# Kernel tuning notes

Measured on AMD Instinct MI355X. Metric: run time of the kernel, lower is better.

Reference implementation:

```python
import jax, jax.numpy as jnp
import numpy as np

NUM_CODES = 4096
CODE_DIM = 512
BETA = 0.25
EPS = 1e-5


def setup_inputs() -> dict:
    key = jax.random.key(0)
    k1, k2 = jax.random.split(key)
    z_e = jax.random.normal(k1, (8, 2048, CODE_DIM), dtype=jnp.float32)
    mask = jnp.ones((8, 2048), dtype=bool)
    # torch init: uniform(-1/num_codes, 1/num_codes)
    codebook = jax.random.uniform(
        k2, (NUM_CODES, CODE_DIM), dtype=jnp.float32,
        minval=-1.0 / NUM_CODES, maxval=1.0 / NUM_CODES)
    return {"z_e": z_e, "mask": mask, "codebook": codebook}


def _l2norm(x, eps=1e-8):
    # matches F.normalize: x / norm.clamp_min(eps)
    n = jnp.sqrt(jnp.sum(x * x, axis=-1, keepdims=True))
    return x / jnp.maximum(n, eps)


def reference(z_e, mask, codebook):
    """Eval-mode forward of VectorQuantizerEMA (no gumbel noise, no code
    dropout, no EMA/restart buffer updates -- those only run in training)."""
    B, L, C = z_e.shape
    K = codebook.shape[0]
    flat = z_e.reshape(-1, C)                      # [N, C]
    fmask = mask.reshape(-1)                       # [N] bool
    mf = fmask.astype(flat.dtype)

    # cosine similarity logits  [N, K]
    logits = _l2norm(flat) @ _l2norm(codebook).T
    logits = jnp.clip(
        jnp.nan_to_num(logits, nan=0.0, posinf=1e9, neginf=-1e9), -60.0, 60.0)

    hard_idx = jnp.argmax(logits, axis=1)          # [N]

    # hard one-hot quantization == gather of codebook rows; masked rows -> 0
    z_q_flat = codebook[hard_idx] * mf[:, None]
    z_q = z_q_flat.reshape(B, L, C)
    z_q_st = z_e + jax.lax.stop_gradient(z_q - z_e)

    m = mf.reshape(B, L, 1)
    valid = jnp.maximum(jnp.sum(m), 1.0)
    commitment_loss = jnp.sum((z_q - jax.lax.stop_gradient(z_e)) ** 2 * m) / valid
    vq_loss = BETA * commitment_loss

    # perplexity over valid assignments (bincount)
    counts = jax.ops.segment_sum(mf, hard_idx, num_segments=K)
    probs = counts / (jnp.sum(counts) + EPS)
    perplexity = jnp.exp(-jnp.sum(probs * jnp.log(probs + EPS)))

    return (z_q, z_q_st, hard_idx.reshape(B, L), vq_loss,
            commitment_loss, perplexity)
```

## Files before the change

kernel.cpp:

```cpp
#include <hip/hip_runtime.h>

typedef __attribute__((ext_vector_type(4))) float f32x4_t;
typedef __attribute__((ext_vector_type(8))) short bf16x8_t;

#define NROWS 16384
#define NCODES 4096
#define DIM 512
#define DELTA 0.005f

#define WS_A      0u
#define WS_B      16777216u
#define WS_TOPE   20971520u
#define WS_COUNTS 37748736u
#define WS_FLAGS  37765120u
#define WS_IDX    37765184u
#define WS_CPART  39206976u

#define OUT_ZQ      0
#define OUT_ZQST    8388608
#define OUT_IDX     16777216
#define OUT_VQ      16793600
#define OUT_COMMIT  16793601
#define OUT_PERP    16793602

__device__ __forceinline__ unsigned short f2bf(float x) {
  unsigned u = __builtin_bit_cast(unsigned, x);
  unsigned r = (u + 0x7FFFu + ((u >> 16) & 1u)) >> 16;
  return (unsigned short)r;
}
__device__ __forceinline__ unsigned hz(unsigned x) {
  return (x - 0x01010101u) & ~x & 0x80808080u;
}
__device__ __forceinline__ unsigned swz64(int r, int u) {
  return (unsigned)(r * 128 + ((u ^ (r & 7)) << 4));
}

__global__ void prep_kernel(const float* __restrict__ z, const float* __restrict__ cb,
                            const uint4* __restrict__ mk,
                            unsigned char* __restrict__ Aws, unsigned char* __restrict__ Bws,
                            unsigned* __restrict__ counts, unsigned* __restrict__ flags) {
  if (blockIdx.x < 16) {
    counts[blockIdx.x * 256 + threadIdx.x] = 0;
  }
  if (blockIdx.x == 0) {
    if (threadIdx.x < 4) flags[threadIdx.x] = 0;
    __syncthreads();
    unsigned f = 0;
    for (int i = threadIdx.x; i < 1024; i += 256) {
      uint4 v = mk[i];
      f |= hz(v.x) | hz(v.y) | hz(v.z) | hz(v.w);
    }
    if (f) atomicOr(&flags[0], 1u);
  }
  const int wv = threadIdx.x >> 6, lane = threadIdx.x & 63;
  const int row = blockIdx.x * 4 + wv;
  if (row >= NROWS + NCODES) return;
  const bool isA = row < NROWS;
  const int lrow = isA ? row : row - NROWS;
  const float* src = (isA ? z : cb) + (size_t)lrow * DIM;
  f32x4_t a = *(const f32x4_t*)(src + lane * 8);
  f32x4_t b = *(const f32x4_t*)(src + lane * 8 + 4);
  double s = 0.0;
#pragma unroll
  for (int e = 0; e < 4; ++e) s += (double)a[e] * a[e] + (double)b[e] * b[e];
#pragma unroll
  for (int off = 1; off < 64; off <<= 1) s += __shfl_xor(s, off);
  const float inv = (float)(1.0 / fmax(sqrt(s), 1e-8));
  union { unsigned short u[8]; uint4 v; } H;
#pragma unroll
  for (int e = 0; e < 4; ++e) {
    H.u[e] = f2bf(a[e] * inv);
    H.u[4 + e] = f2bf(b[e] * inv);
  }
  const int tb = lrow >> 7, rr = lrow & 127;
  const int st = lane >> 3, u = lane & 7;
  unsigned char* chunk = (isA ? Aws : Bws) + ((size_t)tb * 8 + st) * 16384;
  *(uint4*)(chunk + swz64(rr, u)) = H.v;
}

__global__ __launch_bounds__(256, 4) void gemm_p1_kernel(
    const unsigned char* __restrict__ Aws, const unsigned char* __restrict__ Bws,
    float4* __restrict__ topE) {
  __align__(16) __shared__ unsigned char smem[32768];

  const int tid = threadIdx.x;
  const int bid = blockIdx.x;
  const int xcd = bid & 7, q = bid >> 3;
  const int rb = xcd * 16 + (q >> 3), cg = q & 7;
  const int wave = tid >> 6, lane = tid & 63;
  const int wr = wave >> 1, wc = wave & 1;
  const int kg = lane >> 4, lr = lane & 15;

  const unsigned char* Ach = Aws + (size_t)rb * 8 * 16384;

  auto issue_stage = [&](const unsigned char* Asrc, const unsigned char* Bsrc) {
#pragma unroll
    for (int i = 0; i < 8; ++i) {
      const int j = wave * 8 + i;
      const unsigned char* sp = (j < 16) ? (Asrc + (size_t)j * 1024 + lane * 16)
                                         : (Bsrc + (size_t)(j - 16) * 1024 + lane * 16);
      __builtin_amdgcn_global_load_lds(
          (const __attribute__((address_space(1))) void*)sp,
          (__attribute__((address_space(3))) void*)(smem + j * 1024), 16, 0, 0);
    }
  };

  for (int ct = 0; ct < 4; ++ct) {
    const int ctile = cg * 4 + ct;
    const int code0 = ctile * 128;
    const unsigned char* Bch = Bws + (size_t)ctile * 8 * 16384;

    f32x4_t acc[4][4];
#pragma unroll
    for (int m = 0; m < 4; ++m)
#pragma unroll
      for (int n = 0; n < 4; ++n) acc[m][n] = (f32x4_t){0.f, 0.f, 0.f, 0.f};

    for (int st = 0; st < 8; ++st) {
      if (!(st == 0 && ct > 0))
        issue_stage(Ach + (size_t)st * 16384, Bch + (size_t)st * 16384);
      __syncthreads();

#pragma unroll
      for (int kk = 0; kk < 2; ++kk) {
        bf16x8_t ah[4], bh[4];
        const int u = kk * 4 + kg;
#pragma unroll
        for (int m = 0; m < 4; ++m) {
          const int r = wr * 64 + m * 16 + lr;
          ah[m] = *(const bf16x8_t*)(smem + swz64(r, u));
        }
#pragma unroll
        for (int n = 0; n < 4; ++n) {
          const int r = wc * 64 + n * 16 + lr;
          bh[n] = *(const bf16x8_t*)(smem + 16384 + swz64(r, u));
        }
#pragma unroll
        for (int m = 0; m < 4; ++m)
#pragma unroll
          for (int n = 0; n < 4; ++n)
            acc[m][n] = __builtin_amdgcn_mfma_f32_16x16x32_bf16(ah[m], bh[n], acc[m][n], 0, 0, 0);
      }
      __syncthreads();
    }

    if (ct < 3)
      issue_stage(Ach, Bws + (size_t)(ctile + 1) * 8 * 16384);

#pragma unroll
    for (int m = 0; m < 4; ++m) {
#pragma unroll
      for (int j = 0; j < 4; ++j) {
        float v1 = -3e38f, v2 = -3e38f; int i1 = 0, i2 = 0;
#pragma unroll
        for (int n = 0; n < 4; ++n) {
          float v = acc[m][n][j];
          int gc = code0 + wc * 64 + n * 16 + lr;
          if (v > v1) { v2 = v1; i2 = i1; v1 = v; i1 = gc; }
          else if (v > v2) { v2 = v; i2 = gc; }
        }
#pragma unroll
        for (int mask = 1; mask <= 8; mask <<= 1) {
          float ov1 = __shfl_xor(v1, mask); int oi1 = __shfl_xor(i1, mask);
          float ov2 = __shfl_xor(v2, mask); int oi2 = __shfl_xor(i2, mask);
          bool of = (ov1 > v1) || (ov1 == v1 && oi1 < i1);
          float w1 = of ? ov1 : v1;  int k1 = of ? oi1 : i1;
          float lv = of ? v1 : ov1;  int li = of ? i1 : oi1;
          float sv = of ? ov2 : v2;  int si = of ? oi2 : i2;
          bool lw = (lv > sv) || (lv == sv && li < si);
          v1 = w1; i1 = k1;
          v2 = lw ? lv : sv; i2 = lw ? li : si;
        }
        if (lr == m * 4 + j) {
          const int row = rb * 128 + wr * 64 + m * 16 + kg * 4 + j;
          topE[(size_t)row * 64 + ctile * 2 + wc] =
              make_float4(v1, __builtin_bit_cast(float, i1), v2, __builtin_bit_cast(float, i2));
        }
      }
    }
  }
}

__global__ void resolve_referee_kernel(const float* __restrict__ z, const float* __restrict__ cb,
                                       const float4* __restrict__ topE, int* __restrict__ idxf) {
  const int wv = threadIdx.x >> 6, lane = threadIdx.x & 63;
  const int row = blockIdx.x * 4 + wv;
  const float4 qv = topE[(size_t)row * 64 + lane];
  const int myi = __builtin_bit_cast(int, qv.y);
  float bv = qv.x; int bidx = myi;
#pragma unroll
  for (int off = 1; off < 64; off <<= 1) {
    float ov = __shfl_xor(bv, off);
    int oi = __shfl_xor(bidx, off);
    if (ov > bv || (ov == bv && oi < bidx)) { bv = ov; bidx = oi; }
  }
  const float T = bv - 2.0f * DELTA;
  const unsigned long long cmask = __ballot(qv.x >= T);
  const unsigned long long smask = __ballot(qv.z >= T);
  if (__popcll(cmask) <= 1 && smask == 0ull) {
    if (lane == 0) idxf[row] = bidx;
    return;
  }
  const float* zr = z + (size_t)row * DIM + lane * 8;
  double zv[8];
#pragma unroll
  for (int j = 0; j < 8; ++j) zv[j] = (double)zr[j];
  double bs = -1e300; int bi = 1 << 30;
  auto score2 = [&](int k0, int k1) {
    const float* c0 = cb + (size_t)k0 * DIM + lane * 8;
    const float* c1 = cb + (size_t)((k1 < 0) ? k0 : k1) * DIM + lane * 8;
    double d0 = 0, n0 = 0, d1 = 0, n1 = 0;
#pragma unroll
    for (int j = 0; j < 8; ++j) {
      double a = c0[j]; d0 += zv[j] * a; n0 += a * a;
      double b = c1[j]; d1 += zv[j] * b; n1 += b * b;
    }
#pragma unroll
    for (int off = 1; off < 64; off <<= 1) {
      d0 += __shfl_xor(d0, off); n0 += __shfl_xor(n0, off);
      d1 += __shfl_xor(d1, off); n1 += __shfl_xor(n1, off);
    }
    double s0 = d0 / sqrt(n0);
    if (s0 > bs || (s0 == bs && k0 < bi)) { bs = s0; bi = k0; }
    if (k1 >= 0) {
      double s1 = d1 / sqrt(n1);
      if (s1 > bs || (s1 == bs && k1 < bi)) { bs = s1; bi = k1; }
    }
  };
  unsigned long long em = cmask & ~smask;
  while (em) {
    const int h0 = __builtin_ctzll(em); em &= em - 1;
    const int c0 = __shfl(myi, h0);
    int c1 = -1;
    if (em) { const int h1 = __builtin_ctzll(em); em &= em - 1; c1 = __shfl(myi, h1); }
    score2(c0, c1);
  }
  unsigned long long m = smask;
  while (m) {
    const int g = __builtin_ctzll(m); m &= m - 1;
    const int base = g * 64;
    for (int k = 0; k < 64; k += 2) score2(base + k, base + k + 1);
  }
  if (lane == 0) idxf[row] = bi;
}

__global__ void outputs_kernel(const float* __restrict__ z, const float* __restrict__ cb,
                               const unsigned char* __restrict__ mask8, const int* __restrict__ mask32,
                               const unsigned* __restrict__ flags, const int* __restrict__ idxf,
                               float* __restrict__ out, unsigned* __restrict__ counts,
                               double* __restrict__ cpart) {
  __shared__ double wsum[4];
  const int wv = threadIdx.x >> 6, lane = threadIdx.x & 63;
  const int row = blockIdx.x * 4 + wv;
  int idx = idxf[row];
  idx = (idx < 0) ? 0 : ((idx > NCODES - 1) ? NCODES - 1 : idx);
  const int mi = flags[0] ? (mask32[row] != 0) : (mask8[row] != 0);
  const float mf = mi ? 1.0f : 0.0f;
  const float* zr = z + (size_t)row * DIM;
  const float* cr = cb + (size_t)idx * DIM;
  double cs = 0.0;
#pragma unroll
  for (int h = 0; h < 2; ++h) {
    const int j = h * 256 + lane * 4;
    f32x4_t c  = *(const f32x4_t*)(cr + j);
    f32x4_t ze = *(const f32x4_t*)(zr + j);
    f32x4_t zq, zs;
#pragma unroll
    for (int e = 0; e < 4; ++e) {
      float qv = c[e] * mf;
      float d = qv - ze[e];
      zq[e] = qv;
      zs[e] = ze[e] + d;
      cs += (double)(d * d) * mf;
    }
    *(f32x4_t*)(out + OUT_ZQ   + (size_t)row * DIM + j) = zq;
    *(f32x4_t*)(out + OUT_ZQST + (size_t)row * DIM + j) = zs;
  }
#pragma unroll
  for (int off = 32; off; off >>= 1) cs += __shfl_down(cs, off);
  if (lane == 0) {
    wsum[wv] = cs;
    out[OUT_IDX + row] = (float)idx;
    if (mi) atomicAdd(&counts[idx], 1u);
  }
  __syncthreads();
  if (threadIdx.x == 0) cpart[blockIdx.x] = wsum[0] + wsum[1] + wsum[2] + wsum[3];
}

__global__ void finalize_kernel(const double* __restrict__ cpart, const unsigned* __restrict__ counts,
                                float* __restrict__ out) {
  __shared__ double sd[256];
  const int t = threadIdx.x;
  double s = 0;
  for (int i = t; i < 4096; i += 256) s += cpart[i];
  sd[t] = s; __syncthreads();
  for (int off = 128; off; off >>= 1) { if (t < off) sd[t] += sd[t + off]; __syncthreads(); }
  const double commit_sum = sd[0];
  __syncthreads();
  double c = 0;
  for (int i = t; i < 4096; i += 256) c += (double)counts[i];
  sd[t] = c; __syncthreads();
  for (int off = 128; off; off >>= 1) { if (t < off) sd[t] += sd[t + off]; __syncthreads(); }
  const double totc = sd[0];
  __syncthreads();
  const double denom = totc + 1e-5;
  double ent = 0;
  for (int i = t; i < 4096; i += 256) {
    double p = (double)counts[i] / denom;
    ent -= p * log(p + 1e-5);
  }
  sd[t] = ent; __syncthreads();
  for (int off = 128; off; off >>= 1) { if (t < off) sd[t] += sd[t + off]; __syncthreads(); }
  if (t == 0) {
    const double valid = fmax(totc, 1.0);
    const double commitment = commit_sum / valid;
    out[OUT_VQ]     = (float)(0.25 * commitment);
    out[OUT_COMMIT] = (float)commitment;
    out[OUT_PERP]   = (float)exp(sd[0]);
  }
}

extern "C" void kernel_launch(void* const* d_in, const int* in_sizes, int n_in,
                              void* d_out, int out_size, void* d_ws, size_t ws_size,
                              hipStream_t stream) {
  const float* z  = (const float*)d_in[0];
  const void*  mk = d_in[1];
  const float* cb = (const float*)d_in[2];
  float* out = (float*)d_out;
  char* ws = (char*)d_ws;

  unsigned char* Aws    = (unsigned char*)(ws + WS_A);
  unsigned char* Bws    = (unsigned char*)(ws + WS_B);
  float4*        topE   = (float4*)(ws + WS_TOPE);
  unsigned*      counts = (unsigned*)(ws + WS_COUNTS);
  unsigned*      flags  = (unsigned*)(ws + WS_FLAGS);
  int*           idxf   = (int*)(ws + WS_IDX);
  double*        cpart  = (double*)(ws + WS_CPART);

  prep_kernel<<<(NROWS + NCODES) / 4, 256, 0, stream>>>(z, cb, (const uint4*)mk, Aws, Bws,
                                                        counts, flags);
  gemm_p1_kernel<<<1024, 256, 0, stream>>>(Aws, Bws, topE);
  resolve_referee_kernel<<<NROWS / 4, 256, 0, stream>>>(z, cb, topE, idxf);
  outputs_kernel<<<NROWS / 4, 256, 0, stream>>>(z, cb, (const unsigned char*)mk, (const int*)mk,
                                                flags, idxf, out, counts, cpart);
  finalize_kernel<<<1, 256, 0, stream>>>(cpart, counts, out);
}
```

Measured before the change: 311.6 us.

## Accumulate per-lane top-2 across code tiles before cross-lane reduction

The GEMM epilogue no longer does a full 16-lane shuffle top-2 reduction after every 128-code tile. Each lane now keeps a running top-1/top-2 per row in registers across all four code tiles. At the end it does a single 4-lane shuffle reduction, and the second-best index is dropped. The candidate groups written to topE are reorganized into interleaved code sets, and the referee kernel's fallback rescoring loop is updated to enumerate the matching strided codes. This cuts the shuffle work in the epilogue, but adds 48 live registers per thread under launch_bounds(256,4), which risks spills.

```diff
diff --git a/kernel.cpp b/kernel.cpp
--- a/kernel.cpp
+++ b/kernel.cpp
@@ -85,8 +85,8 @@
 
   const int tid = threadIdx.x;
   const int bid = blockIdx.x;
-  const int xcd = bid & 7, q = bid >> 3;
-  const int rb = xcd * 16 + (q >> 3), cg = q & 7;
+  const int xcd = bid & 7, q0 = bid >> 3;
+  const int rb = xcd * 16 + (q0 >> 3), cg = q0 & 7;
   const int wave = tid >> 6, lane = tid & 63;
   const int wr = wave >> 1, wc = wave & 1;
   const int kg = lane >> 4, lr = lane & 15;
@@ -105,6 +105,10 @@
     }
   };
 
+  float tv1[16], tv2[16]; int ti1[16];
+#pragma unroll
+  for (int q = 0; q < 16; ++q) { tv1[q] = -3e38f; tv2[q] = -3e38f; ti1[q] = 0; }
+
   for (int ct = 0; ct < 4; ++ct) {
     const int ctile = cg * 4 + ct;
     const int code0 = ctile * 128;
@@ -148,37 +152,43 @@
       issue_stage(Ach, Bws + (size_t)(ctile + 1) * 8 * 16384);
 
 #pragma unroll
-    for (int m = 0; m < 4; ++m) {
+    for (int m = 0; m < 4; ++m)
 #pragma unroll
       for (int j = 0; j < 4; ++j) {
-        float v1 = -3e38f, v2 = -3e38f; int i1 = 0, i2 = 0;
+        const int q = m * 4 + j;
 #pragma unroll
         for (int n = 0; n < 4; ++n) {
           float v = acc[m][n][j];
           int gc = code0 + wc * 64 + n * 16 + lr;
-          if (v > v1) { v2 = v1; i2 = i1; v1 = v; i1 = gc; }
-          else if (v > v2) { v2 = v; i2 = gc; }
-        }
-#pragma unroll
-        for (int mask = 1; mask <= 8; mask <<= 1) {
-          float ov1 = __shfl_xor(v1, mask); int oi1 = __shfl_xor(i1, mask);
-          float ov2 = __shfl_xor(v2, mask); int oi2 = __shfl_xor(i2, mask);
-          bool of = (ov1 > v1) || (ov1 == v1 && oi1 < i1);
-          float w1 = of ? ov1 : v1;  int k1 = of ? oi1 : i1;
-          float lv = of ? v1 : ov1;  int li = of ? i1 : oi1;
-          float sv = of ? ov2 : v2;  int si = of ? oi2 : i2;
-          bool lw = (lv > sv) || (lv == sv && li < si);
-          v1 = w1; i1 = k1;
-          v2 = lw ? lv : sv; i2 = lw ? li : si;
-        }
-        if (lr == m * 4 + j) {
-          const int row = rb * 128 + wr * 64 + m * 16 + kg * 4 + j;
-          topE[(size_t)row * 64 + ctile * 2 + wc] =
-              make_float4(v1, __builtin_bit_cast(float, i1), v2, __builtin_bit_cast(float, i2));
+          if (v > tv1[q]) { tv2[q] = tv1[q]; tv1[q] = v; ti1[q] = gc; }
+          else if (v > tv2[q]) tv2[q] = v;
         }
       }
-    }
-  }
+  }
+
+#pragma unroll
+  for (int m = 0; m < 4; ++m)
+#pragma unroll
+    for (int j = 0; j < 4; ++j) {
+      const int q = m * 4 + j;
+      float v1 = tv1[q], v2 = tv2[q]; int i1 = ti1[q];
+#pragma unroll
+      for (int mask = 1; mask <= 2; mask <<= 1) {
+        float ov1 = __shfl_xor(v1, mask); int oi1 = __shfl_xor(i1, mask);
+        float ov2 = __shfl_xor(v2, mask);
+        bool of = (ov1 > v1) || (ov1 == v1 && oi1 < i1);
+        float w1 = of ? ov1 : v1;  int k1 = of ? oi1 : i1;
+        float lv = of ? v1 : ov1;
+        float sv = of ? ov2 : v2;
+        v1 = w1; i1 = k1;
+        v2 = (lv > sv) ? lv : sv;
+      }
+      if ((lr & 3) == 0) {
+        const int row = rb * 128 + wr * 64 + m * 16 + kg * 4 + j;
+        topE[(size_t)row * 64 + cg * 8 + wc * 4 + (lr >> 2)] =
+            make_float4(v1, __builtin_bit_cast(float, i1), v2, 0.f);
+      }
+    }
 }
 
 __global__ void resolve_referee_kernel(const float* __restrict__ z, const float* __restrict__ cb,
@@ -238,8 +248,13 @@
   unsigned long long m = smask;
   while (m) {
     const int g = __builtin_ctzll(m); m &= m - 1;
-    const int base = g * 64;
-    for (int k = 0; k < 64; k += 2) score2(base + k, base + k + 1);
+    const int cbase = (g >> 3) * 512 + ((g >> 2) & 1) * 64 + (g & 3) * 4;
+    for (int w = 0; w < 64; w += 2) {
+      const int k0 = cbase + (w >> 4) * 128 + ((w >> 2) & 3) * 16 + (w & 3);
+      const int w1 = w + 1;
+      const int k1 = cbase + (w1 >> 4) * 128 + ((w1 >> 2) & 3) * 16 + (w1 & 3);
+      score2(k0, k1);
+    }
   }
   if (lane == 0) idxf[row] = bi;
 }
```

Result: no change. 308.8 us (-0.9%).
